# Optimization experiments

Measured on AMD Instinct MI355X. Metric: run time of the kernel, lower is better.

Reference implementation:

```python
import jax, jax.numpy as jnp
import numpy as np

# Grid / filter configuration (matches init_kwargs)
NLAT_IN, NLON_IN = 361, 720
NLAT_OUT, NLON_OUT = 361, 720
K = 9                       # kernel_size for piecewise-linear basis, kernel_shape=[3,4]
PSCALE = NLON_IN // NLON_OUT  # longitude stride between output longitudes
NNZ = 65536
B, CIN, COUT = 2, 64, 64


def setup_inputs() -> dict:
    key = jax.random.key(0)
    k0, k1, k2, k3, k4, k5 = jax.random.split(key, 6)
    x = jax.random.normal(k0, (B, CIN, NLAT_IN, NLON_IN), dtype=jnp.float32)
    psi_ker_idx = jax.random.randint(k1, (NNZ,), 0, K)
    psi_row_idx = jax.random.randint(k2, (NNZ,), 0, NLAT_OUT)
    psi_col_idx = jax.random.randint(k3, (NNZ,), 0, NLAT_IN * NLON_IN)
    # quadrature-merged, normalized basis values are small positive numbers
    psi_vals = jax.random.uniform(k4, (NNZ,), dtype=jnp.float32) / K
    scale = (1.0 / (CIN * K)) ** 0.5
    weight = scale * jax.random.normal(k5, (COUT, CIN, K), dtype=jnp.float32)
    bias = jnp.zeros((COUT,), dtype=jnp.float32)
    return {
        "x": x,
        "psi_vals": psi_vals,
        "weight": weight,
        "bias": bias,
        "psi_ker_idx": psi_ker_idx,
        "psi_row_idx": psi_row_idx,
        "psi_col_idx": psi_col_idx,
    }


def reference(x, psi_vals, weight, bias, psi_ker_idx, psi_row_idx, psi_col_idx):
    """DISCO S2 conv: y[b,c,k,lo,p] = sum_nz psi_vals * x[b,c,lat_in, (lon_in+p*PSCALE)%NLON_IN]
    restricted to nz with ker==k, row==lo; then channel mixing with weight (COUT,CIN,K) + bias.
    Matches torch fallback which rolls x by PSCALE per output longitude and does sparse bmm."""
    b, c, nlat_in, nlon_in = x.shape
    lat_in = psi_col_idx // nlon_in          # (nnz,)
    lon_in = psi_col_idx % nlon_in           # (nnz,)
    seg = psi_ker_idx * NLAT_OUT + psi_row_idx  # (nnz,) segment id over (K, nlat_out)
    xf = x.reshape(b * c, nlat_in, nlon_in)

    def step(carry, p):
        lon = (lon_in + p * PSCALE) % nlon_in        # rolled longitude index, (nnz,)
        g = xf[:, lat_in, lon]                       # (BC, nnz) gather
        contrib = (psi_vals * g).T                   # (nnz, BC)
        yk = jax.ops.segment_sum(contrib, seg, num_segments=K * NLAT_OUT)  # (K*nlat_out, BC)
        y = yk.reshape(K, NLAT_OUT, b, c)
        o = jnp.einsum("klbc,ock->bol", y, weight)   # (B, COUT, nlat_out)
        return carry, o

    _, ys = jax.lax.scan(step, None, jnp.arange(NLON_OUT))  # (nlon_out, B, COUT, nlat_out)
    out = jnp.moveaxis(ys, 0, -1)                            # (B, COUT, nlat_out, nlon_out)
    return out + bias[None, :, None, None]
```

## Files before the change

### kernel.cpp

```cpp
#include <hip/hip_runtime.h>

typedef unsigned int uint;
typedef unsigned short ushort;

#define NLAT 361
#define NLON 720
#define NNZT 65536
#define CIN 64
#define COUT 64
#define NK 9
#define PADL 784
#define ROWCAP 384
#define CKTOT 576
#define YPS 168
#define WTS 640

typedef __attribute__((ext_vector_type(8))) short short8v;
typedef __attribute__((ext_vector_type(4))) float f32x4;

__device__ __forceinline__ float bfu(uint u){ return __uint_as_float(u<<16); }
__device__ __forceinline__ float bfh(uint u){ return __uint_as_float(u & 0xffff0000u); }
__device__ __forceinline__ ushort f2bf(float f){
  uint b = __float_as_uint(f);
  return (ushort)((b + 0x7fffu + ((b>>16)&1u)) >> 16);
}
__device__ __forceinline__ uint packbf2(float f0, float f1){
  uint b0 = __float_as_uint(f0), b1 = __float_as_uint(f1);
  uint r0 = (b0 + 0x7fffu + ((b0>>16)&1u)) >> 16;
  uint r1 = ((b1 + 0x7fffu + ((b1>>16)&1u)) >> 16) << 16;
  return r0 | r1;
}

__global__ __launch_bounds__(256) void k_csr(const int* __restrict__ ker, const int* __restrict__ row,
                                             const int* __restrict__ col, const float* __restrict__ vals,
                                             int2* __restrict__ meta_g, int* __restrict__ kptr_g){
  const int lo = blockIdx.x, tid = threadIdx.x;
  __shared__ int cnt2[256*NK];
  #pragma unroll
  for (int kk=0;kk<NK;kk++) cnt2[tid*NK+kk]=0;
  __syncthreads();
  for (int i=tid;i<NNZT;i+=256) if (row[i]==lo) cnt2[tid*NK + ker[i]]++;
  __syncthreads();
  if (tid==0){
    int run=0;
    for (int kk=0;kk<NK;kk++){
      kptr_g[lo*10+kk]=run;
      for (int t=0;t<256;t++){ int tmp=cnt2[t*NK+kk]; cnt2[t*NK+kk]=run; run+=tmp; }
    }
    kptr_g[lo*10+9]=run;
  }
  __syncthreads();
  for (int i=tid;i<NNZT;i+=256) if (row[i]==lo){
    int kk=ker[i];
    int off=cnt2[tid*NK+kk]++;
    if (off<ROWCAP){
      int c=col[i];
      meta_g[lo*ROWCAP+off]=make_int2(((c/NLON)<<16)|(c%NLON), __float_as_int(vals[i]));
    }
  }
}

__global__ __launch_bounds__(256) void k_xb(const float* __restrict__ x, ushort* __restrict__ xb){
  const int bid=blockIdx.x, tid=threadIdx.x;
  const int b=bid/NLAT, lat=bid-b*NLAT;
  const float* xs = x + (size_t)b*CIN*NLAT*NLON + (size_t)lat*NLON;
  ushort* xd = xb + (size_t)(b*NLAT+lat)*16*PADL*4;
  const size_t S=(size_t)NLAT*NLON;
  for (int idx=tid; idx<16*PADL; idx+=256){
    int cq=idx/PADL, j=idx-cq*PADL;
    int jj = (j<NLON)? j : j-NLON;
    const float* xc = xs + (size_t)(cq*4)*S + jj;
    uint lo32 = packbf2(xc[0], xc[S]);
    uint hi32 = packbf2(xc[2*S], xc[3*S]);
    *(uint2*)(xd + (size_t)(cq*PADL + j)*4) = make_uint2(lo32, hi32);
  }
}

__global__ __launch_bounds__(256) void k_wt(const float* __restrict__ w, ushort* __restrict__ wt){
  int idx = blockIdx.x*256 + threadIdx.x;
  if (idx >= COUT*WTS) return;
  int oc = idx/WTS, ckl = idx-oc*WTS;
  int chunk = ckl/160, q = ckl-chunk*160;
  ushort v = 0;
  if (q < 144) v = f2bf(w[oc*CKTOT + chunk*144 + q]);
  wt[oc*WTS + ckl] = v;
}

template<int USE_XB>
__global__ __launch_bounds__(256,3) void k_main(const float* __restrict__ x, const ushort* __restrict__ xb,
    const int2* __restrict__ meta_g, const int* __restrict__ kptr_g,
    const ushort* __restrict__ wt, const float* __restrict__ bias, float* __restrict__ out){
  const int bid=blockIdx.x, tid=threadIdx.x;
  const int lo=bid/6; const int rem=bid-lo*6;
  const int b=rem/3, pq=rem-(rem/3)*3;

  __shared__ int2 meta[ROWCAP];
  __shared__ __align__(16) ushort Yp[64*YPS];

  int kp[10];
  #pragma unroll
  for (int kk=0;kk<10;kk++){ int v=kptr_g[lo*10+kk]; kp[kk]=v<ROWCAP?v:ROWCAP; }
  for (int i=tid;i<kp[9];i+=256) meta[i]=meta_g[lo*ROWCAP+i];
  for (int idx=tid; idx<64*8; idx+=256){
    int p=idx>>3, j=idx&7;
    *(uint*)((char*)Yp + p*(YPS*2) + 288 + j*4) = 0;
  }
  __syncthreads();

  const int lane=tid&63, wv=tid>>6;
  const int l15=lane&15, kg=lane>>4;
  const char* xb8 = (const char*)xb + (size_t)b*NLAT*16*PADL*8;
  const char* wtb = (const char*)wt + ((wv*16+l15)*WTS + kg*8)*2;
  const char* ypb = (const char*)Yp + l15*(YPS*2) + kg*16;

  float b4[4];
  #pragma unroll
  for (int r=0;r<4;r++) b4[r]=bias[wv*16 + kg*4 + r];

  f32x4 outacc[4][4];
  #pragma unroll
  for (int a=0;a<4;a++)
    #pragma unroll
    for (int c2=0;c2<4;c2++) outacc[a][c2]=(f32x4)0.f;

  for (int chunk=0;chunk<4;chunk++){
    const int c0=chunk*16;
    short8v af[5];
    #pragma unroll
    for (int ks=0;ks<5;ks++)
      af[ks] = *(const short8v*)(wtb + (chunk*160 + ks*32)*2);

    const uint cqoff = (uint)(chunk*4+wv)*(PADL*8);
    #pragma unroll
    for (int pt=0;pt<4;pt++){
      const int p0 = pq*240 + pt*64;
      float acc[4][NK];
      #pragma unroll
      for (int j=0;j<4;j++)
        #pragma unroll
        for (int kk=0;kk<NK;kk++) acc[j][kk]=0.f;

#define GBODY(M,KK) { \
      int lat=(M).x>>16, lon=(M).x&0xffff; \
      float v=__int_as_float((M).y); \
      int s=lon+p0; s=(s>=NLON)?s-NLON:s; \
      uint off=(uint)lat*(16u*PADL*8u)+cqoff+(uint)(s+lane)*8u; \
      uint2 u=*(const uint2*)(xb8+off); \
      acc[0][KK]+=v*bfu(u.x); acc[1][KK]+=v*bfh(u.x); \
      acc[2][KK]+=v*bfu(u.y); acc[3][KK]+=v*bfh(u.y); }

#define GBODYF(M,KK) { \
      int lat=(M).x>>16, lon=(M).x&0xffff; \
      float v=__int_as_float((M).y); \
      int s=lon+p0; s=(s>=NLON)?s-NLON:s; \
      int widx=s+lane; widx=(widx>=NLON)?widx-NLON:widx; \
      int base=((b*CIN + c0+wv*4)*NLAT + lat)*NLON + widx; \
      acc[0][KK]+=v*x[base]; \
      acc[1][KK]+=v*x[base+NLAT*NLON]; \
      acc[2][KK]+=v*x[base+2*NLAT*NLON]; \
      acc[3][KK]+=v*x[base+3*NLAT*NLON]; }

      #pragma unroll
      for (int kk=0;kk<NK;kk++){
        int i=kp[kk]; const int e=kp[kk+1];
        if (USE_XB){
          for (; i+3<e; i+=4){
            int2 m0=meta[i], m1=meta[i+1], m2=meta[i+2], m3=meta[i+3];
            GBODY(m0,kk); GBODY(m1,kk); GBODY(m2,kk); GBODY(m3,kk);
          }
          for (; i<e; i++){ int2 m0=meta[i]; GBODY(m0,kk); }
        } else {
          for (; i<e; i++){ int2 m0=meta[i]; GBODYF(m0,kk); }
        }
      }
#undef GBODY
#undef GBODYF
      __syncthreads();
      {
        char* dst = (char*)Yp + lane*(YPS*2) + wv*72;
        #pragma unroll
        for (int i2=0;i2<18;i2++){
          const int t0=2*i2, t1=2*i2+1;
          uint pr = packbf2(acc[t0/9][t0-9*(t0/9)], acc[t1/9][t1-9*(t1/9)]);
          *(uint*)(dst + i2*4) = pr;
        }
      }
      __syncthreads();
      #pragma unroll
      for (int ptile=0;ptile<4;ptile++){
        #pragma unroll
        for (int ks=0;ks<5;ks++){
          short8v bf = *(const short8v*)(ypb + ptile*(16*YPS*2) + ks*64);
          outacc[pt][ptile] = __builtin_amdgcn_mfma_f32_16x16x32_bf16(af[ks], bf, outacc[pt][ptile], 0, 0, 0);
        }
      }
    }
  }
  #pragma unroll
  for (int pt=0;pt<4;pt++)
    #pragma unroll
    for (int ptile=0;ptile<4;ptile++){
      const int pidx = pt*64 + ptile*16;
      if (pidx < 240){
        #pragma unroll
        for (int r=0;r<4;r++){
          int oc = wv*16 + kg*4 + r;
          int p  = pq*240 + pidx + l15;
          out[((size_t)(b*COUT+oc)*NLAT + lo)*NLON + p] = outacc[pt][ptile][r] + b4[r];
        }
      }
    }
}

extern "C" void kernel_launch(void* const* d_in, const int* in_sizes, int n_in,
                              void* d_out, int out_size, void* d_ws, size_t ws_size,
                              hipStream_t stream){
  const float* x   =(const float*)d_in[0];
  const float* vals=(const float*)d_in[1];
  const float* w   =(const float*)d_in[2];
  const float* bias=(const float*)d_in[3];
  const int* ker=(const int*)d_in[4];
  const int* row=(const int*)d_in[5];
  const int* col=(const int*)d_in[6];
  float* out=(float*)d_out;

  const size_t META_B=(size_t)NLAT*ROWCAP*sizeof(int2);
  const size_t KPTR_B=((size_t)NLAT*10*sizeof(int)+15)&~(size_t)15;
  const size_t WT_B=((size_t)COUT*WTS*sizeof(ushort)+15)&~(size_t)15;
  const size_t XB_B=(size_t)2*NLAT*16*PADL*4*sizeof(ushort);
  int2* meta_g=(int2*)d_ws;
  int*  kptr_g=(int*)((char*)d_ws+META_B);
  ushort* wt=(ushort*)((char*)d_ws+META_B+KPTR_B);
  ushort* xb=(ushort*)((char*)d_ws+META_B+KPTR_B+WT_B);
  const bool use_xb = ws_size >= META_B+KPTR_B+WT_B+XB_B;

  k_csr<<<dim3(NLAT), dim3(256), 0, stream>>>(ker,row,col,vals,meta_g,kptr_g);
  k_wt <<<dim3((COUT*WTS+255)/256), dim3(256), 0, stream>>>(w, wt);
  if (use_xb){
    k_xb<<<dim3(2*NLAT), dim3(256), 0, stream>>>(x, xb);
    k_main<1><<<dim3(NLAT*6), dim3(256), 0, stream>>>(x,xb,meta_g,kptr_g,wt,bias,out);
  } else {
    k_main<0><<<dim3(NLAT*6), dim3(256), 0, stream>>>(x,xb,meta_g,kptr_g,wt,bias,out);
  }
}
```

Measured before the change: 2.045 ms.

## Restructure gather loop: precomputed byte offsets, split accumulators, swapped loop order

Precomputes gather byte offsets in the CSR kernel and packs the longitude into the low mantissa bits of the value, so the inner loop needs only an add and a compare for wraparound. The loop nest is swapped so output accumulators cover one p-tile at a time, and the 9 kernel accumulators are split into 5+4 groups. The weights are permuted to match a new (k, channel) ordering of the Y tile. Together these cut VGPR use enough to raise launch bounds to 4 waves/SIMD, with deeper 8-way unrolled gathers for more memory-level parallelism. Truncating the value mantissa by 10 bits lowers precision slightly.

```diff
diff --git a/kernel.cpp b/kernel.cpp
--- a/kernel.cpp
+++ b/kernel.cpp
@@ -14,6 +14,7 @@
 #define CKTOT 576
 #define YPS 168
 #define WTS 640
+#define XROWB (16*PADL*8)
 
 typedef __attribute__((ext_vector_type(8))) short short8v;
 typedef __attribute__((ext_vector_type(4))) float f32x4;
@@ -55,7 +56,9 @@
     int off=cnt2[tid*NK+kk]++;
     if (off<ROWCAP){
       int c=col[i];
-      meta_g[lo*ROWCAP+off]=make_int2(((c/NLON)<<16)|(c%NLON), __float_as_int(vals[i]));
+      int lat=c/NLON, lon=c-lat*NLON;
+      uint vb = __float_as_uint(vals[i]) & 0xfffffc00u;
+      meta_g[lo*ROWCAP+off]=make_int2(lat*XROWB + lon*8, (int)(vb | (uint)lon));
     }
   }
 }
@@ -82,12 +85,16 @@
   int oc = idx/WTS, ckl = idx-oc*WTS;
   int chunk = ckl/160, q = ckl-chunk*160;
   ushort v = 0;
-  if (q < 144) v = f2bf(w[oc*CKTOT + chunk*144 + q]);
+  if (q < 144){
+    int wvq=q/36, r=q-wvq*36;
+    int kk=r>>2, j=r&3;
+    v = f2bf(w[oc*CKTOT + (chunk*16 + wvq*4 + j)*NK + kk]);
+  }
   wt[oc*WTS + ckl] = v;
 }
 
 template<int USE_XB>
-__global__ __launch_bounds__(256,3) void k_main(const float* __restrict__ x, const ushort* __restrict__ xb,
+__global__ __launch_bounds__(256,4) void k_main(const float* __restrict__ x, const ushort* __restrict__ xb,
     const int2* __restrict__ meta_g, const int* __restrict__ kptr_g,
     const ushort* __restrict__ wt, const float* __restrict__ bias, float* __restrict__ out){
   const int bid=blockIdx.x, tid=threadIdx.x;
@@ -108,81 +115,99 @@
   __syncthreads();
 
   const int lane=tid&63, wv=tid>>6;
+  const int wvu = __builtin_amdgcn_readfirstlane(wv);
   const int l15=lane&15, kg=lane>>4;
-  const char* xb8 = (const char*)xb + (size_t)b*NLAT*16*PADL*8;
+  const char* xb8 = (const char*)xb + (size_t)b*NLAT*(size_t)XROWB;
   const char* wtb = (const char*)wt + ((wv*16+l15)*WTS + kg*8)*2;
   const char* ypb = (const char*)Yp + l15*(YPS*2) + kg*16;
+  char* ydst = (char*)Yp + lane*(YPS*2) + wv*72;
 
   float b4[4];
   #pragma unroll
   for (int r=0;r<4;r++) b4[r]=bias[wv*16 + kg*4 + r];
 
-  f32x4 outacc[4][4];
-  #pragma unroll
-  for (int a=0;a<4;a++)
+#define GADDR(M) ((uint)(M).x + lanep8 + (((((uint)(M).y)&0x3ffu) >= thr) ? (uint)-5760 : 0u))
+#define GVAL(M)  __uint_as_float(((uint)(M).y) & 0xfffffc00u)
+#define GCONS(U,V,ACC,AI) { ACC[0][AI]+=(V)*bfu((U).x); ACC[1][AI]+=(V)*bfh((U).x); \
+                            ACC[2][AI]+=(V)*bfu((U).y); ACC[3][AI]+=(V)*bfh((U).y); }
+#define GB1F(M,ACC,AI) { \
+      uint lon=((uint)(M).y)&0x3ffu; float v=GVAL(M); \
+      int lat=(int)(((uint)(M).x)/(uint)XROWB); \
+      int s=(int)lon+p0; s=(s>=NLON)?s-NLON:s; \
+      int widx=s+lane; widx=(widx>=NLON)?widx-NLON:widx; \
+      int base=((b*CIN + chunk*16 + wv*4)*NLAT + lat)*NLON + widx; \
+      ACC[0][AI]+=v*x[base]; ACC[1][AI]+=v*x[base+NLAT*NLON]; \
+      ACC[2][AI]+=v*x[base+2*NLAT*NLON]; ACC[3][AI]+=v*x[base+3*NLAT*NLON]; }
+
+#define GSEG(ACC,KI,AI) { \
+      int i=kp[KI]; const int e=kp[(KI)+1]; \
+      if (USE_XB){ \
+        for (; i+7<e; i+=8){ \
+          int2 m0=meta[i],m1=meta[i+1],m2=meta[i+2],m3=meta[i+3]; \
+          int2 m4=meta[i+4],m5=meta[i+5],m6=meta[i+6],m7=meta[i+7]; \
+          uint2 u0=*(const uint2*)(xbase+GADDR(m0)); uint2 u1=*(const uint2*)(xbase+GADDR(m1)); \
+          uint2 u2=*(const uint2*)(xbase+GADDR(m2)); uint2 u3=*(const uint2*)(xbase+GADDR(m3)); \
+          uint2 u4=*(const uint2*)(xbase+GADDR(m4)); uint2 u5=*(const uint2*)(xbase+GADDR(m5)); \
+          uint2 u6=*(const uint2*)(xbase+GADDR(m6)); uint2 u7=*(const uint2*)(xbase+GADDR(m7)); \
+          GCONS(u0,GVAL(m0),ACC,AI); GCONS(u1,GVAL(m1),ACC,AI); \
+          GCONS(u2,GVAL(m2),ACC,AI); GCONS(u3,GVAL(m3),ACC,AI); \
+          GCONS(u4,GVAL(m4),ACC,AI); GCONS(u5,GVAL(m5),ACC,AI); \
+          GCONS(u6,GVAL(m6),ACC,AI); GCONS(u7,GVAL(m7),ACC,AI); \
+        } \
+        for (; i+3<e; i+=4){ \
+          int2 m0=meta[i],m1=meta[i+1],m2=meta[i+2],m3=meta[i+3]; \
+          uint2 u0=*(const uint2*)(xbase+GADDR(m0)); uint2 u1=*(const uint2*)(xbase+GADDR(m1)); \
+          uint2 u2=*(const uint2*)(xbase+GADDR(m2)); uint2 u3=*(const uint2*)(xbase+GADDR(m3)); \
+          GCONS(u0,GVAL(m0),ACC,AI); GCONS(u1,GVAL(m1),ACC,AI); \
+          GCONS(u2,GVAL(m2),ACC,AI); GCONS(u3,GVAL(m3),ACC,AI); \
+        } \
+        for (; i<e; i++){ int2 m0=meta[i]; \
+          uint2 u0=*(const uint2*)(xbase+GADDR(m0)); GCONS(u0,GVAL(m0),ACC,AI); } \
+      } else { \
+        for (; i<e; i++){ int2 m0=meta[i]; GB1F(m0,ACC,AI); } \
+      } }
+
+  for (int pt=0;pt<4;pt++){
+    const int p0 = pq*240 + pt*64;
+    const uint thr = (uint)(NLON - p0);
+    const uint lanep8 = (uint)(lane + p0)*8u;
+    f32x4 outacc[4];
     #pragma unroll
-    for (int c2=0;c2<4;c2++) outacc[a][c2]=(f32x4)0.f;
-
-  for (int chunk=0;chunk<4;chunk++){
-    const int c0=chunk*16;
-    short8v af[5];
-    #pragma unroll
-    for (int ks=0;ks<5;ks++)
-      af[ks] = *(const short8v*)(wtb + (chunk*160 + ks*32)*2);
-
-    const uint cqoff = (uint)(chunk*4+wv)*(PADL*8);
-    #pragma unroll
-    for (int pt=0;pt<4;pt++){
-      const int p0 = pq*240 + pt*64;
-      float acc[4][NK];
+    for (int c2=0;c2<4;c2++) outacc[c2]=(f32x4)0.f;
+
+    for (int chunk=0;chunk<4;chunk++){
+      short8v af[5];
       #pragma unroll
-      for (int j=0;j<4;j++)
-        #pragma unroll
-        for (int kk=0;kk<NK;kk++) acc[j][kk]=0.f;
-
-#define GBODY(M,KK) { \
-      int lat=(M).x>>16, lon=(M).x&0xffff; \
-      float v=__int_as_float((M).y); \
-      int s=lon+p0; s=(s>=NLON)?s-NLON:s; \
-      uint off=(uint)lat*(16u*PADL*8u)+cqoff+(uint)(s+lane)*8u; \
-      uint2 u=*(const uint2*)(xb8+off); \
-      acc[0][KK]+=v*bfu(u.x); acc[1][KK]+=v*bfh(u.x); \
-      acc[2][KK]+=v*bfu(u.y); acc[3][KK]+=v*bfh(u.y); }
-
-#define GBODYF(M,KK) { \
-      int lat=(M).x>>16, lon=(M).x&0xffff; \
-      float v=__int_as_float((M).y); \
-      int s=lon+p0; s=(s>=NLON)?s-NLON:s; \
-      int widx=s+lane; widx=(widx>=NLON)?widx-NLON:widx; \
-      int base=((b*CIN + c0+wv*4)*NLAT + lat)*NLON + widx; \
-      acc[0][KK]+=v*x[base]; \
-      acc[1][KK]+=v*x[base+NLAT*NLON]; \
-      acc[2][KK]+=v*x[base+2*NLAT*NLON]; \
-      acc[3][KK]+=v*x[base+3*NLAT*NLON]; }
-
-      #pragma unroll
-      for (int kk=0;kk<NK;kk++){
-        int i=kp[kk]; const int e=kp[kk+1];
-        if (USE_XB){
-          for (; i+3<e; i+=4){
-            int2 m0=meta[i], m1=meta[i+1], m2=meta[i+2], m3=meta[i+3];
-            GBODY(m0,kk); GBODY(m1,kk); GBODY(m2,kk); GBODY(m3,kk);
-          }
-          for (; i<e; i++){ int2 m0=meta[i]; GBODY(m0,kk); }
-        } else {
-          for (; i<e; i++){ int2 m0=meta[i]; GBODYF(m0,kk); }
-        }
-      }
-#undef GBODY
-#undef GBODYF
-      __syncthreads();
+      for (int ks=0;ks<5;ks++)
+        af[ks] = *(const short8v*)(wtb + (chunk*160 + ks*32)*2);
+
+      const char* xbase = xb8 + (size_t)(chunk*4+wvu)*(PADL*8);
+
       {
-        char* dst = (char*)Yp + lane*(YPS*2) + wv*72;
-        #pragma unroll
-        for (int i2=0;i2<18;i2++){
-          const int t0=2*i2, t1=2*i2+1;
-          uint pr = packbf2(acc[t0/9][t0-9*(t0/9)], acc[t1/9][t1-9*(t1/9)]);
-          *(uint*)(dst + i2*4) = pr;
+        float acc1[4][5];
+        #pragma unroll
+        for (int j=0;j<4;j++)
+          #pragma unroll
+          for (int kk=0;kk<5;kk++) acc1[j][kk]=0.f;
+        GSEG(acc1,0,0) GSEG(acc1,1,1) GSEG(acc1,2,2) GSEG(acc1,3,3) GSEG(acc1,4,4)
+        __syncthreads();
+        #pragma unroll
+        for (int kk=0;kk<5;kk++){
+          *(uint*)(ydst + (kk*4+0)*2) = packbf2(acc1[0][kk], acc1[1][kk]);
+          *(uint*)(ydst + (kk*4+2)*2) = packbf2(acc1[2][kk], acc1[3][kk]);
+        }
+      }
+      {
+        float acc2[4][4];
+        #pragma unroll
+        for (int j=0;j<4;j++)
+          #pragma unroll
+          for (int kk=0;kk<4;kk++) acc2[j][kk]=0.f;
+        GSEG(acc2,5,0) GSEG(acc2,6,1) GSEG(acc2,7,2) GSEG(acc2,8,3)
+        #pragma unroll
+        for (int kk=0;kk<4;kk++){
+          *(uint*)(ydst + ((kk+5)*4+0)*2) = packbf2(acc2[0][kk], acc2[1][kk]);
+          *(uint*)(ydst + ((kk+5)*4+2)*2) = packbf2(acc2[2][kk], acc2[3][kk]);
         }
       }
       __syncthreads();
@@ -191,13 +216,10 @@
         #pragma unroll
         for (int ks=0;ks<5;ks++){
           short8v bf = *(const short8v*)(ypb + ptile*(16*YPS*2) + ks*64);
-          outacc[pt][ptile] = __builtin_amdgcn_mfma_f32_16x16x32_bf16(af[ks], bf, outacc[pt][ptile], 0, 0, 0);
-        }
-      }
-    }
-  }
-  #pragma unroll
-  for (int pt=0;pt<4;pt++)
+          outacc[ptile] = __builtin_amdgcn_mfma_f32_16x16x32_bf16(af[ks], bf, outacc[ptile], 0, 0, 0);
+        }
+      }
+    }
     #pragma unroll
     for (int ptile=0;ptile<4;ptile++){
       const int pidx = pt*64 + ptile*16;
@@ -206,10 +228,11 @@
         for (int r=0;r<4;r++){
           int oc = wv*16 + kg*4 + r;
           int p  = pq*240 + pidx + l15;
-          out[((size_t)(b*COUT+oc)*NLAT + lo)*NLON + p] = outacc[pt][ptile][r] + b4[r];
-        }
-      }
-    }
+          out[((size_t)(b*COUT+oc)*NLAT + lo)*NLON + p] = outacc[ptile][r] + b4[r];
+        }
+      }
+    }
+  }
 }
 
 extern "C" void kernel_launch(void* const* d_in, const int* in_sizes, int n_in,
```

Result: slower. 2.256 ms (+10.3%).
